# Kernel optimization log

Hardware: AMD Instinct MI355X
Metric: run time of the kernel (lower is better)

The kernel has to match this reference:

```python
import jax, jax.numpy as jnp
import numpy as np

N, E, G = 20000, 100000, 64          # nodes, edges, graphs in batch
IN, HID = 63, 128                    # in_feat, hidden_feat (per-head dim)
HEADS = (8, 8, 8)                    # num_heads per GATv2 layer
NCLS = 18
EPS = 1e-5


def setup_inputs() -> dict:
    key = jax.random.key(0)
    ks = list(jax.random.split(key, 48))
    it = iter(ks)
    nrm = lambda shape, s=0.05: jax.random.normal(next(it), shape, jnp.float32) * s

    inp = {
        "h": jax.random.normal(next(it), (N, IN), jnp.float32),
        "src": jax.random.randint(next(it), (E,), 0, N, dtype=jnp.int32),
        "dst": jax.random.randint(next(it), (E,), 0, N, dtype=jnp.int32),
        "gid": jnp.sort(jax.random.randint(next(it), (N,), 0, G, dtype=jnp.int32)),
    }
    dims = [(IN, HEADS[0] * HID), (HEADS[0] * HID, HEADS[1] * HID), (HEADS[1] * HID, HEADS[2] * HID)]
    for l, (din, dout) in enumerate(dims, 1):
        H = HEADS[l - 1]
        inp[f"w_src{l}"] = nrm((din, dout))
        inp[f"b_src{l}"] = jnp.zeros((dout,), jnp.float32)
        inp[f"w_dst{l}"] = nrm((din, dout))
        inp[f"b_dst{l}"] = jnp.zeros((dout,), jnp.float32)
        inp[f"attn{l}"] = nrm((H, HID))
        inp[f"bias{l}"] = jnp.zeros((dout,), jnp.float32)
        inp[f"gamma{l}"] = jnp.ones((dout,), jnp.float32)
        inp[f"beta{l}"] = jnp.zeros((dout,), jnp.float32)
    inp["fc1_w"] = nrm((HEADS[2] * HID, HID * 8))   # 1024 -> 1024 (hidden_feat*num_heads -> hidden_feat? see note)
    inp["fc1_b"] = jnp.zeros((HID * 8,), jnp.float32)
    inp["fc2_w"] = nrm((HID * 8, 1024))
    inp["fc2_b"] = jnp.zeros((1024,), jnp.float32)
    inp["fc3_w"] = nrm((1024, NCLS))
    inp["fc3_b"] = jnp.zeros((NCLS,), jnp.float32)
    return inp


def _gatv2(h, w_src, b_src, w_dst, b_dst, attn, bias, src, dst):
    """DGL GATv2Conv forward (dropouts are identity in eval mode)."""
    H, D = attn.shape
    fs = (h @ w_src + b_src).reshape(N, H, D)   # [N,H,D]
    fd = (h @ w_dst + b_dst).reshape(N, H, D)
    e = jax.nn.leaky_relu(fs[src] + fd[dst], 0.2)          # [E,H,D], GATv2 negative_slope=0.2
    sc = jnp.einsum('ehd,hd->eh', e, attn)                 # [E,H] attention logits
    m = jax.ops.segment_max(sc, dst, num_segments=N)       # segment-softmax over in-edges
    m = jnp.where(jnp.isfinite(m), m, 0.0)                 # guard isolated nodes
    ex = jnp.exp(sc - m[dst])
    den = jax.ops.segment_sum(ex, dst, num_segments=N)
    alpha = ex / den[dst]                                  # [E,H]
    out = jax.ops.segment_sum(alpha[..., None] * fs[src], dst, num_segments=N)  # [N,H,D]
    return out.reshape(N, H * D) + bias


def _bn(x, gamma, beta):
    mu = x.mean(0)
    var = x.var(0)  # biased, as torch BN uses for normalization
    return (x - mu) * jax.lax.rsqrt(var + EPS) * gamma + beta


def _lrelu(x):
    return jax.nn.leaky_relu(x, 0.01)  # torch F.leaky_relu default slope


def reference(h, src, dst, gid,
              w_src1, b_src1, w_dst1, b_dst1, attn1, bias1, gamma1, beta1,
              w_src2, b_src2, w_dst2, b_dst2, attn2, bias2, gamma2, beta2,
              w_src3, b_src3, w_dst3, b_dst3, attn3, bias3, gamma3, beta3,
              fc1_w, fc1_b, fc2_w, fc2_b, fc3_w, fc3_b):
    x = _lrelu(_bn(_gatv2(h, w_src1, b_src1, w_dst1, b_dst1, attn1, bias1, src, dst), gamma1, beta1))
    x = _lrelu(_bn(_gatv2(x, w_src2, b_src2, w_dst2, b_dst2, attn2, bias2, src, dst), gamma2, beta2))
    x = _lrelu(_bn(_gatv2(x, w_src3, b_src3, w_dst3, b_dst3, attn3, bias3, src, dst), gamma3, beta3))
    # AvgPooling: mean over nodes of each graph
    cnt = jax.ops.segment_sum(jnp.ones((N,), x.dtype), gid, num_segments=G)
    hg = jax.ops.segment_sum(x, gid, num_segments=G) / jnp.maximum(cnt, 1.0)[:, None]  # [G, 1024]
    z = _lrelu(hg @ fc1_w + fc1_b)
    z = _lrelu(z @ fc2_w + fc2_b)
    return z @ fc3_w + fc3_b  # [G, 18]
```

## Files before the change

kernel.cpp:

```cpp
#include <hip/hip_runtime.h>
#include <math.h>

#define N_NODES 20000
#define N_PAD   20096
#define N_EDGES 100000
#define N_GRAPHS 64
#define IN_F 63
#define NHEAD 8
#define F 1024
#define NCLS 18
#define BN_EPS 1e-5f
#define BN_CHUNKS 256

typedef __attribute__((ext_vector_type(8))) _Float16 half8v;
typedef __attribute__((ext_vector_type(4))) _Float16 half4v;
typedef __attribute__((ext_vector_type(4))) float f32x4;

__global__ void k_zero_i32(int* __restrict__ p, int n) {
    int i = blockIdx.x * blockDim.x + threadIdx.x;
    if (i < n) p[i] = 0;
}

__global__ void k_copy_i32(int* __restrict__ d, const int* __restrict__ s, int n) {
    int i = blockIdx.x * blockDim.x + threadIdx.x;
    if (i < n) d[i] = s[i];
}

__global__ void k_count(const int* __restrict__ dst, int* __restrict__ cnt) {
    int i = blockIdx.x * blockDim.x + threadIdx.x;
    if (i < N_EDGES) atomicAdd(&cnt[dst[i]], 1);
}

__global__ void k_scan(const int* __restrict__ cnt, int* __restrict__ off) {
    __shared__ int tsum[256];
    const int CH = (N_NODES + 255) / 256;
    int t = threadIdx.x;
    int s = 0;
    for (int i = 0; i < CH; ++i) {
        int idx = t * CH + i;
        if (idx < N_NODES) s += cnt[idx];
    }
    tsum[t] = s;
    __syncthreads();
    if (t == 0) {
        int acc = 0;
        for (int i = 0; i < 256; ++i) { int v = tsum[i]; tsum[i] = acc; acc += v; }
    }
    __syncthreads();
    int run = tsum[t];
    for (int i = 0; i < CH; ++i) {
        int idx = t * CH + i;
        if (idx < N_NODES) { off[idx] = run; run += cnt[idx]; }
    }
    if (t == 255) off[N_NODES] = run;
}

__global__ void k_fill(const int* __restrict__ dst, int* __restrict__ cursor,
                       int* __restrict__ csr_e) {
    int i = blockIdx.x * blockDim.x + threadIdx.x;
    if (i < N_EDGES) {
        int p = atomicAdd(&cursor[dst[i]], 1);
        csr_e[p] = i;
    }
}

__global__ void k_sort_buckets(const int* __restrict__ off, int* __restrict__ csr_e) {
    int n = blockIdx.x * blockDim.x + threadIdx.x;
    if (n >= N_NODES) return;
    int b = off[n], e = off[n + 1];
    for (int i = b + 1; i < e; ++i) {
        int v = csr_e[i];
        int j = i - 1;
        while (j >= b && csr_e[j] > v) { csr_e[j + 1] = csr_e[j]; --j; }
        csr_e[j + 1] = v;
    }
}

__global__ void k_gstart(const int* __restrict__ gid, int* __restrict__ gstart) {
    int g = blockIdx.x * blockDim.x + threadIdx.x;
    if (g > N_GRAPHS) return;
    int lo = 0, hi = N_NODES;
    while (lo < hi) {
        int mid = (lo + hi) >> 1;
        if (gid[mid] < g) lo = mid + 1; else hi = mid;
    }
    gstart[g] = lo;
}

__global__ void k_cvt_h(const float* __restrict__ h, _Float16* __restrict__ xh) {
    int idx = blockIdx.x * 256 + threadIdx.x;
    if (idx >= N_PAD * 64) return;
    int m = idx >> 6, k = idx & 63;
    float v = (m < N_NODES && k < IN_F) ? h[m * IN_F + k] : 0.f;
    xh[idx] = (_Float16)v;
}

__global__ void k_zero_pad(_Float16* __restrict__ xh) {
    int idx = blockIdx.x * 256 + threadIdx.x;
    const int total = (N_PAD - N_NODES) * F;
    if (idx < total) xh[(size_t)N_NODES * F + idx] = (_Float16)0.f;
}

__global__ void k_cvt_w(const float* __restrict__ W, _Float16* __restrict__ wh,
                        int K, int Kpad) {
    __shared__ float t[32][33];
    int kt = blockIdx.x * 32, nt = blockIdx.y * 32;
    int tx = threadIdx.x & 31, ty = threadIdx.x >> 5;
#pragma unroll
    for (int j = 0; j < 4; ++j) {
        int k = kt + ty + j * 8;
        t[ty + j * 8][tx] = (k < K) ? W[(size_t)k * F + nt + tx] : 0.f;
    }
    __syncthreads();
#pragma unroll
    for (int j = 0; j < 4; ++j) {
        int n = nt + ty + j * 8;
        wh[(size_t)n * Kpad + kt + tx] = (_Float16)t[tx][ty + j * 8];
    }
}

#define AS1C(p) ((const __attribute__((address_space(1))) void*)(p))
#define AS3(p)  ((__attribute__((address_space(3))) void*)(p))

__launch_bounds__(256, 2)
__global__ void k_gemm_dual(const _Float16* __restrict__ A,
                            const _Float16* __restrict__ Bs, const _Float16* __restrict__ Bd,
                            const float* __restrict__ bias_s, const float* __restrict__ bias_d,
                            _Float16* __restrict__ Cs, _Float16* __restrict__ Cd, int Kpad) {
    __shared__ _Float16 lds[24576];
    const int tid = threadIdx.x;
    const int l = tid & 63, w = tid >> 6;

    const int orig = blockIdx.y * 8 + blockIdx.x;
    const int wg = (orig & 7) * (N_PAD / 128) + (orig >> 3);
    const int by = wg >> 3, bx = wg & 7;

    const int grow = w * 32 + (l >> 3);
    const int gcol = ((l & 7) ^ (l >> 3)) << 3;
    const size_t rstep = (size_t)8 * Kpad;
    const _Float16* gA = A + (size_t)(by * 128 + grow) * Kpad + gcol;
    const _Float16* gBs = Bs + (size_t)(bx * 128 + grow) * Kpad + gcol;
    const _Float16* gBd = Bd + (size_t)(bx * 128 + grow) * Kpad + gcol;
    char* sA = (char*)lds + w * 4096;
    char* sBs = (char*)lds + 16384 + w * 4096;
    char* sBd = (char*)lds + 32768 + w * 4096;

    const int wr = (w >> 1) * 64, wc = (w & 1) * 64;
    const int frow = l & 15;
    const int swz = (l & 7) << 4;
    const int kbase = (l >> 4) * 16;

    f32x4 accS[4][4], accD[4][4];
    const f32x4 fzero = {0.f, 0.f, 0.f, 0.f};
#pragma unroll
    for (int i = 0; i < 4; ++i)
#pragma unroll
        for (int j = 0; j < 4; ++j) { accS[i][j] = fzero; accD[i][j] = fzero; }

    for (int k0 = 0; k0 < Kpad; k0 += 64) {
#pragma unroll
        for (int j = 0; j < 4; ++j) {
            __builtin_amdgcn_global_load_lds(AS1C(gA + j * rstep), AS3(sA + j * 1024), 16, 0, 0);
            __builtin_amdgcn_global_load_lds(AS1C(gBs + j * rstep), AS3(sBs + j * 1024), 16, 0, 0);
            __builtin_amdgcn_global_load_lds(AS1C(gBd + j * rstep), AS3(sBd + j * 1024), 16, 0, 0);
        }
        gA += 64; gBs += 64; gBd += 64;
        __syncthreads();

#pragma unroll
        for (int kk = 0; kk < 2; ++kk) {
            const int kb = (kk * 64 + kbase) ^ swz;
            half8v a[4];
#pragma unroll
            for (int mi = 0; mi < 4; ++mi) {
                int row = wr + mi * 16 + frow;
                a[mi] = *(const half8v*)((const char*)lds + row * 128 + kb);
            }
#pragma unroll
            for (int ni = 0; ni < 4; ++ni) {
                int rowb = wc + ni * 16 + frow;
                half8v bs = *(const half8v*)((const char*)lds + 16384 + rowb * 128 + kb);
                half8v bd = *(const half8v*)((const char*)lds + 32768 + rowb * 128 + kb);
#pragma unroll
                for (int mi = 0; mi < 4; ++mi) {
                    accS[mi][ni] = __builtin_amdgcn_mfma_f32_16x16x32_f16(a[mi], bs, accS[mi][ni], 0, 0, 0);
                    accD[mi][ni] = __builtin_amdgcn_mfma_f32_16x16x32_f16(a[mi], bd, accD[mi][ni], 0, 0, 0);
                }
            }
        }
        __syncthreads();
    }

    const int crow0 = by * 128 + wr + (l >> 4) * 4;
    const int ccol = bx * 128 + wc + (l & 15);
    float bS[4], bD[4];
#pragma unroll
    for (int ni = 0; ni < 4; ++ni) { bS[ni] = bias_s[ccol + ni * 16]; bD[ni] = bias_d[ccol + ni * 16]; }
#pragma unroll
    for (int mi = 0; mi < 4; ++mi) {
#pragma unroll
        for (int r = 0; r < 4; ++r) {
            int row = crow0 + mi * 16 + r;
            if (row < N_NODES) {
#pragma unroll
                for (int ni = 0; ni < 4; ++ni) {
                    int col = ccol + ni * 16;
                    Cs[(size_t)row * F + col] = (_Float16)(accS[mi][ni][r] + bS[ni]);
                    Cd[(size_t)row * F + col] = (_Float16)(accD[mi][ni][r] + bD[ni]);
                }
            }
        }
    }
}

__launch_bounds__(256)
__global__ void k_gat(const _Float16* __restrict__ fs, const _Float16* __restrict__ fd,
                      const int* __restrict__ off, const int* __restrict__ csr_e,
                      const int* __restrict__ src, const float* __restrict__ attn,
                      const float* __restrict__ bias, float* __restrict__ y) {
    __shared__ int s_src[256];
    const int n = blockIdx.x;
    const int t = threadIdx.x;
    const int b = off[n], e = off[n + 1];

    half4v fdv = *(const half4v*)(fd + (size_t)n * F + t * 4);
    const float fd0 = (float)fdv.x, fd1 = (float)fdv.y, fd2 = (float)fdv.z, fd3 = (float)fdv.w;
    const float4 av = *(const float4*)(attn + (t >> 5) * 128 + (t & 31) * 4);

    float m = -1e30f, den = 0.f;
    float ax = 0.f, ay = 0.f, az = 0.f, aw = 0.f;

    for (int c0 = b; c0 < e; c0 += 256) {
        int ncur = e - c0; if (ncur > 256) ncur = 256;
        __syncthreads();
        if (t < ncur) s_src[t] = src[csr_e[c0 + t]];
        __syncthreads();
        for (int i = 0; i < ncur; ++i) {
            int s = s_src[i];
            half4v fsv = *(const half4v*)(fs + (size_t)s * F + t * 4);
            float f0 = (float)fsv.x, f1 = (float)fsv.y, f2 = (float)fsv.z, f3 = (float)fsv.w;
            float vx = f0 + fd0; vx = vx > 0.f ? vx : 0.2f * vx;
            float vy = f1 + fd1; vy = vy > 0.f ? vy : 0.2f * vy;
            float vz = f2 + fd2; vz = vz > 0.f ? vz : 0.2f * vz;
            float vw = f3 + fd3; vw = vw > 0.f ? vw : 0.2f * vw;
            float p = vx * av.x + vy * av.y + vz * av.z + vw * av.w;
            p += __shfl_xor(p, 1);
            p += __shfl_xor(p, 2);
            p += __shfl_xor(p, 4);
            p += __shfl_xor(p, 8);
            p += __shfl_xor(p, 16);
            float mn = fmaxf(m, p);
            float so = __expf(m - mn);
            float wexp = __expf(p - mn);
            den = den * so + wexp;
            ax = ax * so + wexp * f0;
            ay = ay * so + wexp * f1;
            az = az * so + wexp * f2;
            aw = aw * so + wexp * f3;
            m = mn;
        }
    }
    float inv = (e > b) ? 1.f / den : 0.f;
    const float4 bb = *(const float4*)(bias + t * 4);
    float4 o;
    o.x = ax * inv + bb.x;
    o.y = ay * inv + bb.y;
    o.z = az * inv + bb.z;
    o.w = aw * inv + bb.w;
    *(float4*)(y + (size_t)n * F + t * 4) = o;
}

__global__ void k_bnpart(const float* __restrict__ y, float* __restrict__ part) {
    const int ROWS = (N_NODES + BN_CHUNKS - 1) / BN_CHUNKS;
    int blk = blockIdx.x;
    int t = threadIdx.x;
    int r0 = blk * ROWS;
    int r1 = r0 + ROWS; if (r1 > N_NODES) r1 = N_NODES;
    float sx = 0.f, sy = 0.f, sz = 0.f, sw = 0.f;
    float qx = 0.f, qy = 0.f, qz = 0.f, qw = 0.f;
    for (int r = r0; r < r1; ++r) {
        float4 v = *(const float4*)(y + (size_t)r * F + t * 4);
        sx += v.x; sy += v.y; sz += v.z; sw += v.w;
        qx += v.x * v.x; qy += v.y * v.y; qz += v.z * v.z; qw += v.w * v.w;
    }
    float4 s4; s4.x = sx; s4.y = sy; s4.z = sz; s4.w = sw;
    float4 q4; q4.x = qx; q4.y = qy; q4.z = qz; q4.w = qw;
    *(float4*)(part + (size_t)blk * (2 * F) + t * 4) = s4;
    *(float4*)(part + (size_t)blk * (2 * F) + F + t * 4) = q4;
}

__global__ void k_bnfin(const float* __restrict__ part, const float* __restrict__ gamma,
                        const float* __restrict__ beta, float* __restrict__ scale,
                        float* __restrict__ shift) {
    int c = blockIdx.x * blockDim.x + threadIdx.x;
    if (c >= F) return;
    float s = 0.f, q = 0.f;
    for (int b = 0; b < BN_CHUNKS; ++b) {
        s += part[(size_t)b * (2 * F) + c];
        q += part[(size_t)b * (2 * F) + F + c];
    }
    float mu = s / (float)N_NODES;
    float var = q / (float)N_NODES - mu * mu;
    float sc = gamma[c] * rsqrtf(var + BN_EPS);
    scale[c] = sc;
    shift[c] = beta[c] - mu * sc;
}

__global__ void k_bnapply(const float* __restrict__ y, const float* __restrict__ scale,
                          const float* __restrict__ shift, float* __restrict__ x,
                          _Float16* __restrict__ xh, int mode) {
    int i = blockIdx.x * blockDim.x + threadIdx.x;
    if (i >= N_NODES * (F / 4)) return;
    int c4 = (i & (F / 4 - 1)) * 4;
    float4 v = ((const float4*)y)[i];
    float4 o;
    o.x = v.x * scale[c4 + 0] + shift[c4 + 0];
    o.y = v.y * scale[c4 + 1] + shift[c4 + 1];
    o.z = v.z * scale[c4 + 2] + shift[c4 + 2];
    o.w = v.w * scale[c4 + 3] + shift[c4 + 3];
    o.x = o.x > 0.f ? o.x : 0.01f * o.x;
    o.y = o.y > 0.f ? o.y : 0.01f * o.y;
    o.z = o.z > 0.f ? o.z : 0.01f * o.z;
    o.w = o.w > 0.f ? o.w : 0.01f * o.w;
    if (mode == 0) {
        half4v h4;
        h4.x = (_Float16)o.x; h4.y = (_Float16)o.y;
        h4.z = (_Float16)o.z; h4.w = (_Float16)o.w;
        *(half4v*)&xh[(size_t)i * 4] = h4;
    } else {
        ((float4*)x)[i] = o;
    }
}

__global__ void k_pool(const float* __restrict__ x, const int* __restrict__ gstart,
                       _Float16* __restrict__ hg16) {
    int g = blockIdx.y;
    int col = blockIdx.x * 256 + threadIdx.x;
    int r0 = gstart[g], r1 = gstart[g + 1];
    float s = 0.f;
    for (int r = r0; r < r1; ++r) s += x[(size_t)r * F + col];
    float inv = (r1 > r0) ? 1.f / (float)(r1 - r0) : 0.f;
    hg16[(size_t)g * F + col] = (_Float16)(s * inv);
}

__launch_bounds__(256)
__global__ void k_mlp_mfma(const _Float16* __restrict__ A16, const _Float16* __restrict__ Bt,
                           const float* __restrict__ bias, _Float16* __restrict__ out16,
                           float* __restrict__ out32, int mode) {
    const int l = threadIdx.x & 63, w = threadIdx.x >> 6;
    const int bx = blockIdx.x;
    const int fko = (l >> 4) * 8;

    const _Float16* pa = A16 + (size_t)(w * 16 + (l & 15)) * 1024 + fko;
    const _Float16* pb = Bt + (size_t)(bx * 64 + (l & 15)) * 1024 + fko;

    f32x4 acc[4];
    const f32x4 fzero = {0.f, 0.f, 0.f, 0.f};
#pragma unroll
    for (int ni = 0; ni < 4; ++ni) acc[ni] = fzero;

#pragma unroll 4
    for (int k0 = 0; k0 < 1024; k0 += 32) {
        half8v a = *(const half8v*)(pa + k0);
#pragma unroll
        for (int ni = 0; ni < 4; ++ni) {
            half8v b = *(const half8v*)(pb + (size_t)ni * 16 * 1024 + k0);
            acc[ni] = __builtin_amdgcn_mfma_f32_16x16x32_f16(a, b, acc[ni], 0, 0, 0);
        }
    }

    const int row0 = w * 16 + (l >> 4) * 4;
    const int col0 = bx * 64 + (l & 15);
#pragma unroll
    for (int ni = 0; ni < 4; ++ni) {
        int col = col0 + ni * 16;
        float bb = bias[col];
#pragma unroll
        for (int r = 0; r < 4; ++r) {
            float v = acc[ni][r] + bb;
            v = v > 0.f ? v : 0.01f * v;
            if (mode == 0) out16[(size_t)(row0 + r) * 1024 + col] = (_Float16)v;
            else out32[(size_t)(row0 + r) * 1024 + col] = v;
        }
    }
}

__global__ void k_fc3(const float* __restrict__ z2, const float* __restrict__ W,
                      const float* __restrict__ b, float* __restrict__ out) {
    int gw = (blockIdx.x * blockDim.x + threadIdx.x) >> 6;
    int lane = threadIdx.x & 63;
    if (gw >= N_GRAPHS * NCLS) return;
    int row = gw / NCLS, col = gw - row * NCLS;
    float s = 0.f;
    for (int k = lane; k < 1024; k += 64) s += z2[(size_t)row * 1024 + k] * W[(size_t)k * NCLS + col];
#pragma unroll
    for (int o = 32; o; o >>= 1) s += __shfl_down(s, o);
    if (lane == 0) out[(size_t)row * NCLS + col] = s + b[col];
}

extern "C" void kernel_launch(void* const* d_in, const int* in_sizes, int n_in,
                              void* d_out, int out_size, void* d_ws, size_t ws_size,
                              hipStream_t stream) {
    const float* h = (const float*)d_in[0];
    const int* src = (const int*)d_in[1];
    const int* dst = (const int*)d_in[2];
    const int* gid = (const int*)d_in[3];

    const float *w_src[3], *b_src[3], *w_dst[3], *b_dst[3], *attn[3], *bias[3], *gamma[3], *beta[3];
    for (int l = 0; l < 3; ++l) {
        int base = 4 + l * 8;
        w_src[l] = (const float*)d_in[base + 0];
        b_src[l] = (const float*)d_in[base + 1];
        w_dst[l] = (const float*)d_in[base + 2];
        b_dst[l] = (const float*)d_in[base + 3];
        attn[l]  = (const float*)d_in[base + 4];
        bias[l]  = (const float*)d_in[base + 5];
        gamma[l] = (const float*)d_in[base + 6];
        beta[l]  = (const float*)d_in[base + 7];
    }
    const float* fc1_w = (const float*)d_in[28];
    const float* fc1_b = (const float*)d_in[29];
    const float* fc2_w = (const float*)d_in[30];
    const float* fc2_b = (const float*)d_in[31];
    const float* fc3_w = (const float*)d_in[32];
    const float* fc3_b = (const float*)d_in[33];

    char* base = (char*)d_ws;
    size_t o = 0;
    auto carve = [&](size_t bytes) -> char* {
        char* p = base + o;
        o += (bytes + 255) & ~(size_t)255;
        return p;
    };
    _Float16* fs16 = (_Float16*)carve((size_t)N_NODES * F * 2);
    _Float16* fd16 = (_Float16*)carve((size_t)N_NODES * F * 2);
    float* y = (float*)carve((size_t)N_NODES * F * 4);
    _Float16* xh = (_Float16*)carve((size_t)N_PAD * F * 2);
    _Float16* wsh = (_Float16*)carve((size_t)F * F * 2);
    _Float16* wdh = (_Float16*)carve((size_t)F * F * 2);
    _Float16* fc1h = (_Float16*)carve((size_t)F * F * 2);
    _Float16* fc2h = (_Float16*)carve((size_t)F * F * 2);
    int* cnt = (int*)carve((size_t)N_NODES * 4);
    int* off = (int*)carve((size_t)(N_NODES + 1) * 4);
    int* cursor = (int*)carve((size_t)N_NODES * 4);
    int* csr_e = (int*)carve((size_t)N_EDGES * 4);
    float* part = (float*)carve((size_t)BN_CHUNKS * 2 * F * 4);
    float* scale = (float*)carve(F * 4);
    float* shift = (float*)carve(F * 4);
    int* gstart = (int*)carve((N_GRAPHS + 1) * 4);
    _Float16* hg16 = (_Float16*)carve((size_t)N_GRAPHS * F * 2);
    _Float16* z1h = (_Float16*)carve((size_t)N_GRAPHS * F * 2);
    float* z2 = (float*)carve((size_t)N_GRAPHS * F * 4);
    (void)ws_size;

    k_zero_i32<<<(N_NODES + 255) / 256, 256, 0, stream>>>(cnt, N_NODES);
    k_count<<<(N_EDGES + 255) / 256, 256, 0, stream>>>(dst, cnt);
    k_scan<<<1, 256, 0, stream>>>(cnt, off);
    k_copy_i32<<<(N_NODES + 255) / 256, 256, 0, stream>>>(cursor, off, N_NODES);
    k_fill<<<(N_EDGES + 255) / 256, 256, 0, stream>>>(dst, cursor, csr_e);
    k_sort_buckets<<<(N_NODES + 255) / 256, 256, 0, stream>>>(off, csr_e);
    k_gstart<<<1, 128, 0, stream>>>(gid, gstart);

    k_cvt_h<<<(N_PAD * 64 + 255) / 256, 256, 0, stream>>>(h, xh);
    k_zero_pad<<<((N_PAD - N_NODES) * F + 255) / 256, 256, 0, stream>>>(xh);
    k_cvt_w<<<dim3(F / 32, F / 32), 256, 0, stream>>>(fc1_w, fc1h, F, F);
    k_cvt_w<<<dim3(F / 32, F / 32), 256, 0, stream>>>(fc2_w, fc2h, F, F);

    const dim3 ggrid(8, N_PAD / 128);
    for (int l = 0; l < 3; ++l) {
        const int K = (l == 0) ? IN_F : F;
        const int Kp = (l == 0) ? 64 : F;
        k_cvt_w<<<dim3(Kp / 32, F / 32), 256, 0, stream>>>(w_src[l], wsh, K, Kp);
        k_cvt_w<<<dim3(Kp / 32, F / 32), 256, 0, stream>>>(w_dst[l], wdh, K, Kp);
        k_gemm_dual<<<ggrid, 256, 0, stream>>>(xh, wsh, wdh, b_src[l], b_dst[l], fs16, fd16, Kp);
        k_gat<<<N_NODES, 256, 0, stream>>>(fs16, fd16, off, csr_e, src, attn[l], bias[l], y);
        k_bnpart<<<BN_CHUNKS, 256, 0, stream>>>(y, part);
        k_bnfin<<<F / 256, 256, 0, stream>>>(part, gamma[l], beta[l], scale, shift);
        k_bnapply<<<(N_NODES * (F / 4) + 255) / 256, 256, 0, stream>>>(
            y, scale, shift, y, xh, (l == 2) ? 1 : 0);
    }

    k_pool<<<dim3(4, N_GRAPHS), 256, 0, stream>>>(y, gstart, hg16);
    k_mlp_mfma<<<16, 256, 0, stream>>>(hg16, fc1h, fc1_b, z1h, nullptr, 0);
    k_mlp_mfma<<<16, 256, 0, stream>>>(z1h, fc2h, fc2_b, nullptr, z2, 1);
    k_fc3<<<(N_GRAPHS * NCLS * 64 + 255) / 256, 256, 0, stream>>>(z2, fc3_w, fc3_b, (float*)d_out);
}
```

Measured before the change: 851.0 us.

## Double-buffer GEMM B tiles, load A from global, store GAT output in fp16

The dual GEMM now reads A fragments straight from global memory into registers and stages only the B tiles through LDS, double-buffered, so the next tile's loads overlap the current tile's MFMAs and one barrier per step is removed. The GAT output buffer y changes from fp32 to fp16, halving traffic for the GAT store, the BN statistics pass and the BN apply pass. The two weight-conversion launches per layer are merged into one launch with a z dimension. The risks are uncoalesced, non-shared A loads from global memory and lost precision in the BN inputs from the fp16 intermediate.

```diff
diff --git a/kernel.cpp b/kernel.cpp
--- a/kernel.cpp
+++ b/kernel.cpp
@@ -101,8 +101,11 @@
     if (idx < total) xh[(size_t)N_NODES * F + idx] = (_Float16)0.f;
 }
 
-__global__ void k_cvt_w(const float* __restrict__ W, _Float16* __restrict__ wh,
-                        int K, int Kpad) {
+__global__ void k_cvt_w2(const float* __restrict__ W0, _Float16* __restrict__ o0,
+                         const float* __restrict__ W1, _Float16* __restrict__ o1,
+                         int K, int Kpad) {
+    const float* W = blockIdx.z ? W1 : W0;
+    _Float16* wh = blockIdx.z ? o1 : o0;
     __shared__ float t[32][33];
     int kt = blockIdx.x * 32, nt = blockIdx.y * 32;
     int tx = threadIdx.x & 31, ty = threadIdx.x >> 5;
@@ -127,9 +130,8 @@
                             const _Float16* __restrict__ Bs, const _Float16* __restrict__ Bd,
                             const float* __restrict__ bias_s, const float* __restrict__ bias_d,
                             _Float16* __restrict__ Cs, _Float16* __restrict__ Cd, int Kpad) {
-    __shared__ _Float16 lds[24576];
-    const int tid = threadIdx.x;
-    const int l = tid & 63, w = tid >> 6;
+    __shared__ _Float16 lds[2][2][128 * 64];
+    const int l = threadIdx.x & 63, w = threadIdx.x >> 6;
 
     const int orig = blockIdx.y * 8 + blockIdx.x;
     const int wg = (orig & 7) * (N_PAD / 128) + (orig >> 3);
@@ -138,18 +140,16 @@
     const int grow = w * 32 + (l >> 3);
     const int gcol = ((l & 7) ^ (l >> 3)) << 3;
     const size_t rstep = (size_t)8 * Kpad;
-    const _Float16* gA = A + (size_t)(by * 128 + grow) * Kpad + gcol;
     const _Float16* gBs = Bs + (size_t)(bx * 128 + grow) * Kpad + gcol;
     const _Float16* gBd = Bd + (size_t)(bx * 128 + grow) * Kpad + gcol;
-    char* sA = (char*)lds + w * 4096;
-    char* sBs = (char*)lds + 16384 + w * 4096;
-    char* sBd = (char*)lds + 32768 + w * 4096;
 
     const int wr = (w >> 1) * 64, wc = (w & 1) * 64;
     const int frow = l & 15;
     const int swz = (l & 7) << 4;
     const int kbase = (l >> 4) * 16;
 
+    const _Float16* pA = A + (size_t)(by * 128 + wr + frow) * Kpad + (l >> 4) * 8;
+
     f32x4 accS[4][4], accD[4][4];
     const f32x4 fzero = {0.f, 0.f, 0.f, 0.f};
 #pragma unroll
@@ -157,38 +157,49 @@
 #pragma unroll
         for (int j = 0; j < 4; ++j) { accS[i][j] = fzero; accD[i][j] = fzero; }
 
+    auto stage = [&](int b, int k0) {
+        char* ds = (char*)&lds[b][0][0] + w * 4096;
+        char* dd = (char*)&lds[b][1][0] + w * 4096;
+#pragma unroll
+        for (int j = 0; j < 4; ++j) {
+            __builtin_amdgcn_global_load_lds(AS1C(gBs + k0 + j * rstep), AS3(ds + j * 1024), 16, 0, 0);
+            __builtin_amdgcn_global_load_lds(AS1C(gBd + k0 + j * rstep), AS3(dd + j * 1024), 16, 0, 0);
+        }
+    };
+
+    stage(0, 0);
+    __syncthreads();
+
+    int buf = 0;
     for (int k0 = 0; k0 < Kpad; k0 += 64) {
-#pragma unroll
-        for (int j = 0; j < 4; ++j) {
-            __builtin_amdgcn_global_load_lds(AS1C(gA + j * rstep), AS3(sA + j * 1024), 16, 0, 0);
-            __builtin_amdgcn_global_load_lds(AS1C(gBs + j * rstep), AS3(sBs + j * 1024), 16, 0, 0);
-            __builtin_amdgcn_global_load_lds(AS1C(gBd + j * rstep), AS3(sBd + j * 1024), 16, 0, 0);
-        }
-        gA += 64; gBs += 64; gBd += 64;
-        __syncthreads();
-
+        half8v a[4][2];
+#pragma unroll
+        for (int mi = 0; mi < 4; ++mi)
+#pragma unroll
+            for (int kk = 0; kk < 2; ++kk)
+                a[mi][kk] = *(const half8v*)(pA + (size_t)mi * 16 * Kpad + k0 + kk * 32);
+
+        if (k0 + 64 < Kpad) stage(buf ^ 1, k0 + 64);
+
+        const char* lbs = (const char*)&lds[buf][0][0];
+        const char* lbd = (const char*)&lds[buf][1][0];
 #pragma unroll
         for (int kk = 0; kk < 2; ++kk) {
             const int kb = (kk * 64 + kbase) ^ swz;
-            half8v a[4];
-#pragma unroll
-            for (int mi = 0; mi < 4; ++mi) {
-                int row = wr + mi * 16 + frow;
-                a[mi] = *(const half8v*)((const char*)lds + row * 128 + kb);
-            }
 #pragma unroll
             for (int ni = 0; ni < 4; ++ni) {
                 int rowb = wc + ni * 16 + frow;
-                half8v bs = *(const half8v*)((const char*)lds + 16384 + rowb * 128 + kb);
-                half8v bd = *(const half8v*)((const char*)lds + 32768 + rowb * 128 + kb);
+                half8v bs = *(const half8v*)(lbs + rowb * 128 + kb);
+                half8v bd = *(const half8v*)(lbd + rowb * 128 + kb);
 #pragma unroll
                 for (int mi = 0; mi < 4; ++mi) {
-                    accS[mi][ni] = __builtin_amdgcn_mfma_f32_16x16x32_f16(a[mi], bs, accS[mi][ni], 0, 0, 0);
-                    accD[mi][ni] = __builtin_amdgcn_mfma_f32_16x16x32_f16(a[mi], bd, accD[mi][ni], 0, 0, 0);
+                    accS[mi][ni] = __builtin_amdgcn_mfma_f32_16x16x32_f16(a[mi][kk], bs, accS[mi][ni], 0, 0, 0);
+                    accD[mi][ni] = __builtin_amdgcn_mfma_f32_16x16x32_f16(a[mi][kk], bd, accD[mi][ni], 0, 0, 0);
                 }
             }
         }
         __syncthreads();
+        buf ^= 1;
     }
 
     const int crow0 = by * 128 + wr + (l >> 4) * 4;
@@ -217,7 +228,7 @@
 __global__ void k_gat(const _Float16* __restrict__ fs, const _Float16* __restrict__ fd,
                       const int* __restrict__ off, const int* __restrict__ csr_e,
                       const int* __restrict__ src, const float* __restrict__ attn,
-                      const float* __restrict__ bias, float* __restrict__ y) {
+                      const float* __restrict__ bias, _Float16* __restrict__ y16) {
     __shared__ int s_src[256];
     const int n = blockIdx.x;
     const int t = threadIdx.x;
@@ -262,15 +273,15 @@
     }
     float inv = (e > b) ? 1.f / den : 0.f;
     const float4 bb = *(const float4*)(bias + t * 4);
-    float4 o;
-    o.x = ax * inv + bb.x;
-    o.y = ay * inv + bb.y;
-    o.z = az * inv + bb.z;
-    o.w = aw * inv + bb.w;
-    *(float4*)(y + (size_t)n * F + t * 4) = o;
-}
-
-__global__ void k_bnpart(const float* __restrict__ y, float* __restrict__ part) {
+    half4v o;
+    o.x = (_Float16)(ax * inv + bb.x);
+    o.y = (_Float16)(ay * inv + bb.y);
+    o.z = (_Float16)(az * inv + bb.z);
+    o.w = (_Float16)(aw * inv + bb.w);
+    *(half4v*)(y16 + (size_t)n * F + t * 4) = o;
+}
+
+__global__ void k_bnpart(const _Float16* __restrict__ y16, float* __restrict__ part) {
     const int ROWS = (N_NODES + BN_CHUNKS - 1) / BN_CHUNKS;
     int blk = blockIdx.x;
     int t = threadIdx.x;
@@ -279,9 +290,10 @@
     float sx = 0.f, sy = 0.f, sz = 0.f, sw = 0.f;
     float qx = 0.f, qy = 0.f, qz = 0.f, qw = 0.f;
     for (int r = r0; r < r1; ++r) {
-        float4 v = *(const float4*)(y + (size_t)r * F + t * 4);
-        sx += v.x; sy += v.y; sz += v.z; sw += v.w;
-        qx += v.x * v.x; qy += v.y * v.y; qz += v.z * v.z; qw += v.w * v.w;
+        half4v v = *(const half4v*)(y16 + (size_t)r * F + t * 4);
+        float vx = (float)v.x, vy = (float)v.y, vz = (float)v.z, vw = (float)v.w;
+        sx += vx; sy += vy; sz += vz; sw += vw;
+        qx += vx * vx; qy += vy * vy; qz += vz * vz; qw += vw * vw;
     }
     float4 s4; s4.x = sx; s4.y = sy; s4.z = sz; s4.w = sw;
     float4 q4; q4.x = qx; q4.y = qy; q4.z = qz; q4.w = qw;
@@ -306,18 +318,18 @@
     shift[c] = beta[c] - mu * sc;
 }
 
-__global__ void k_bnapply(const float* __restrict__ y, const float* __restrict__ scale,
+__global__ void k_bnapply(const _Float16* __restrict__ y16, const float* __restrict__ scale,
                           const float* __restrict__ shift, float* __restrict__ x,
                           _Float16* __restrict__ xh, int mode) {
     int i = blockIdx.x * blockDim.x + threadIdx.x;
     if (i >= N_NODES * (F / 4)) return;
     int c4 = (i & (F / 4 - 1)) * 4;
-    float4 v = ((const float4*)y)[i];
+    half4v v = ((const half4v*)y16)[i];
     float4 o;
-    o.x = v.x * scale[c4 + 0] + shift[c4 + 0];
-    o.y = v.y * scale[c4 + 1] + shift[c4 + 1];
-    o.z = v.z * scale[c4 + 2] + shift[c4 + 2];
-    o.w = v.w * scale[c4 + 3] + shift[c4 + 3];
+    o.x = (float)v.x * scale[c4 + 0] + shift[c4 + 0];
+    o.y = (float)v.y * scale[c4 + 1] + shift[c4 + 1];
+    o.z = (float)v.z * scale[c4 + 2] + shift[c4 + 2];
+    o.w = (float)v.w * scale[c4 + 3] + shift[c4 + 3];
     o.x = o.x > 0.f ? o.x : 0.01f * o.x;
     o.y = o.y > 0.f ? o.y : 0.01f * o.y;
     o.z = o.z > 0.f ? o.z : 0.01f * o.z;
@@ -434,7 +446,8 @@
     };
     _Float16* fs16 = (_Float16*)carve((size_t)N_NODES * F * 2);
     _Float16* fd16 = (_Float16*)carve((size_t)N_NODES * F * 2);
-    float* y = (float*)carve((size_t)N_NODES * F * 4);
+    _Float16* y16 = (_Float16*)carve((size_t)N_NODES * F * 2);
+    float* x32 = (float*)carve((size_t)N_NODES * F * 4);
     _Float16* xh = (_Float16*)carve((size_t)N_PAD * F * 2);
     _Float16* wsh = (_Float16*)carve((size_t)F * F * 2);
     _Float16* wdh = (_Float16*)carve((size_t)F * F * 2);
@@ -463,24 +476,22 @@
 
     k_cvt_h<<<(N_PAD * 64 + 255) / 256, 256, 0, stream>>>(h, xh);
     k_zero_pad<<<((N_PAD - N_NODES) * F + 255) / 256, 256, 0, stream>>>(xh);
-    k_cvt_w<<<dim3(F / 32, F / 32), 256, 0, stream>>>(fc1_w, fc1h, F, F);
-    k_cvt_w<<<dim3(F / 32, F / 32), 256, 0, stream>>>(fc2_w, fc2h, F, F);
+    k_cvt_w2<<<dim3(F / 32, F / 32, 2), 256, 0, stream>>>(fc1_w, fc1h, fc2_w, fc2h, F, F);
 
     const dim3 ggrid(8, N_PAD / 128);
     for (int l = 0; l < 3; ++l) {
         const int K = (l == 0) ? IN_F : F;
         const int Kp = (l == 0) ? 64 : F;
-        k_cvt_w<<<dim3(Kp / 32, F / 32), 256, 0, stream>>>(w_src[l], wsh, K, Kp);
-        k_cvt_w<<<dim3(Kp / 32, F / 32), 256, 0, stream>>>(w_dst[l], wdh, K, Kp);
+        k_cvt_w2<<<dim3(Kp / 32, F / 32, 2), 256, 0, stream>>>(w_src[l], wsh, w_dst[l], wdh, K, Kp);
         k_gemm_dual<<<ggrid, 256, 0, stream>>>(xh, wsh, wdh, b_src[l], b_dst[l], fs16, fd16, Kp);
-        k_gat<<<N_NODES, 256, 0, stream>>>(fs16, fd16, off, csr_e, src, attn[l], bias[l], y);
-        k_bnpart<<<BN_CHUNKS, 256, 0, stream>>>(y, part);
+        k_gat<<<N_NODES, 256, 0, stream>>>(fs16, fd16, off, csr_e, src, attn[l], bias[l], y16);
+        k_bnpart<<<BN_CHUNKS, 256, 0, stream>>>(y16, part);
         k_bnfin<<<F / 256, 256, 0, stream>>>(part, gamma[l], beta[l], scale, shift);
         k_bnapply<<<(N_NODES * (F / 4) + 255) / 256, 256, 0, stream>>>(
-            y, scale, shift, y, xh, (l == 2) ? 1 : 0);
-    }
-
-    k_pool<<<dim3(4, N_GRAPHS), 256, 0, stream>>>(y, gstart, hg16);
+            y16, scale, shift, x32, xh, (l == 2) ? 1 : 0);
+    }
+
+    k_pool<<<dim3(4, N_GRAPHS), 256, 0, stream>>>(x32, gstart, hg16);
     k_mlp_mfma<<<16, 256, 0, stream>>>(hg16, fc1h, fc1_b, z1h, nullptr, 0);
     k_mlp_mfma<<<16, 256, 0, stream>>>(z1h, fc2h, fc2_b, nullptr, z2, 1);
     k_fc3<<<(N_GRAPHS * NCLS * 64 + 255) / 256, 256, 0, stream>>>(z2, fc3_w, fc3_b, (float*)d_out);
```

Result: slower. 880.2 us (+3.4%).
